# Optimization experiments

Hardware: AMD Instinct MI355X
Metric: run time of the kernel (lower is better)

The kernel has to match this reference:

```python
import jax, jax.numpy as jnp
import numpy as np

N_NODES = 200000
N_EDGES = 6400000
NUM_FEATURES = 128


def _glorot(key, fan_in, fan_out):
    return jax.random.normal(key, (fan_in, fan_out), jnp.float32) * (1.0 / np.sqrt(fan_in))


def gcn_conv(x, src, dst, W, b):
    """PyG GCNConv: h = D^{-1/2}(A+I)D^{-1/2} (x @ W) + b, self-loops added."""
    n = x.shape[0]
    ones = jnp.ones(src.shape, x.dtype)
    # degree after adding self-loops: 1 + in-degree (edges flow src -> dst)
    deg = 1.0 + jax.ops.segment_sum(ones, dst, num_segments=n)
    dinv = jax.lax.rsqrt(deg)  # deg >= 1, safe
    h = x @ W  # [n, out]
    norm = dinv[src] * dinv[dst]  # [E]
    msg = h[src] * norm[:, None]
    agg = jax.ops.segment_sum(msg, dst, num_segments=n)
    agg = agg + h * (dinv * dinv)[:, None]  # self-loop contribution
    return agg + b


def setup_inputs() -> dict:
    key = jax.random.key(0)
    ks = jax.random.split(key, 16)
    x = jax.random.normal(ks[0], (N_NODES, NUM_FEATURES), jnp.float32)
    edge_index = jax.random.randint(ks[1], (2, N_EDGES), 0, N_NODES, dtype=jnp.int64)
    params = {
        'W1': _glorot(ks[2], NUM_FEATURES, 64), 'b1': jnp.zeros((64,), jnp.float32),
        'W2': _glorot(ks[3], 64, 32),           'b2': jnp.zeros((32,), jnp.float32),
        'W3': _glorot(ks[4], 32, 16),           'b3': jnp.zeros((16,), jnp.float32),
        'Wsk02': _glorot(ks[5], NUM_FEATURES, 32), 'bsk02': jnp.zeros((32,), jnp.float32),
        'Wsk13': _glorot(ks[6], 64, 16),           'bsk13': jnp.zeros((16,), jnp.float32),
        'Wlin': _glorot(ks[7], 16, 1),             'blin': jnp.zeros((1,), jnp.float32),
    }
    return {'x': x, 'edge_index': edge_index, **params}


def reference(x, edge_index, W1, b1, W2, b2, W3, b3, Wsk02, bsk02, Wsk13, bsk13, Wlin, blin):
    # Dropout is identity in eval mode.
    src, dst = edge_index[0], edge_index[1]
    h1 = jax.nn.relu(gcn_conv(x, src, dst, W1, b1))
    h2 = jax.nn.relu(gcn_conv(h1, src, dst, W2, b2) + x @ Wsk02 + bsk02)
    h3 = jax.nn.relu(gcn_conv(h2, src, dst, W3, b3) + h1 @ Wsk13 + bsk13)
    return jax.nn.sigmoid(h3 @ Wlin + blin)  # [N, 1]
```

## Files before the change

### kernel.cpp

```cpp
#include <hip/hip_runtime.h>
#include <hip/hip_fp16.h>
#include <math.h>

#define MAXB 1024
#define MAXCB 128
#define TILE1 8192
#define SCAT_T 512
#define EPT1 (TILE1 / SCAT_T)
#define LCAP 13568

typedef _Float16 f16x8 __attribute__((ext_vector_type(8)));
typedef float f32x4 __attribute__((ext_vector_type(4)));


__device__ __forceinline__ unsigned int pack_f16(float a, float b) {
    __half2 h = __floats2half2_rn(a, b);
    return *reinterpret_cast<unsigned int*>(&h);
}
__device__ __forceinline__ float f16_lo(unsigned int u) {
    __half2 h = *reinterpret_cast<__half2*>(&u);
    return __low2float(h);
}
__device__ __forceinline__ float f16_hi(unsigned int u) {
    __half2 h = *reinterpret_cast<__half2*>(&u);
    return __high2float(h);
}
__device__ __forceinline__ void acc8(float* a, uint4 u) {
    a[0] += f16_lo(u.x); a[1] += f16_hi(u.x);
    a[2] += f16_lo(u.y); a[3] += f16_hi(u.y);
    a[4] += f16_lo(u.z); a[5] += f16_hi(u.z);
    a[6] += f16_lo(u.w); a[7] += f16_hi(u.w);
}
__device__ __forceinline__ void unpack8(uint4 u, float* v) {
    v[0] = f16_lo(u.x); v[1] = f16_hi(u.x);
    v[2] = f16_lo(u.y); v[3] = f16_hi(u.y);
    v[4] = f16_lo(u.z); v[5] = f16_hi(u.z);
    v[6] = f16_lo(u.w); v[7] = f16_hi(u.w);
}
__device__ __forceinline__ uint4 h2add4(uint4 a, uint4 b) {
    const __half2* pa = reinterpret_cast<const __half2*>(&a);
    const __half2* pb = reinterpret_cast<const __half2*>(&b);
    uint4 r;
    __half2* pr = reinterpret_cast<__half2*>(&r);
#pragma unroll
    for (int i = 0; i < 4; i++) pr[i] = __hadd2(pa[i], pb[i]);
    return r;
}


__device__ __forceinline__ bool detect64(const int* __restrict__ ei) {
    int lane = threadIdx.x & 63;
    unsigned long long m = __ballot(ei[2 * lane + 1] != 0);
    return m == 0ull;
}

__device__ __forceinline__ int load_src(const int* ei, int e, bool is64, int i) {
    return is64 ? ei[2 * i] : ei[i];
}
__device__ __forceinline__ int load_dst(const int* ei, int e, bool is64, int i) {
    return is64 ? ei[2 * e + 2 * i] : ei[e + i];
}


__global__ __launch_bounds__(256) void bin_count(const int* __restrict__ ei, int e,
                                                 int shift, int* __restrict__ gcnt) {
    __shared__ int h[MAXB];
    for (int i = threadIdx.x; i < MAXB; i += 256) h[i] = 0;
    bool is64 = detect64(ei);
    __syncthreads();
    int stride = gridDim.x * 256;
    for (int i = blockIdx.x * 256 + threadIdx.x; i < e; i += stride) {
        int d = load_dst(ei, e, is64, i);
        atomicAdd(&h[d >> shift], 1);
    }
    __syncthreads();
    for (int i = threadIdx.x; i < MAXB; i += 256)
        if (h[i]) atomicAdd(&gcnt[i], h[i]);
}


__global__ void bin_scan_init(const int* __restrict__ gcnt, int nb, int ncb,
                              int* __restrict__ base, int* __restrict__ gcursor,
                              int* __restrict__ gcur1) {
    __shared__ int sh[1024];
    __shared__ int ex[1024];
    int t = threadIdx.x;
    int v = (t < nb) ? gcnt[t] : 0;
    sh[t] = v;
    __syncthreads();
    for (int off = 1; off < 1024; off <<= 1) {
        int x = (t >= off) ? sh[t - off] : 0;
        __syncthreads();
        sh[t] += x;
        __syncthreads();
    }
    int excl = sh[t] - v;
    ex[t] = excl;
    if (t < nb) {
        base[t] = excl;
        gcursor[t] = excl;
        if (t == nb - 1) base[nb] = sh[t];
    }
    __syncthreads();
    if (t < ncb) gcur1[t] = ex[8 * t];
}


__global__ __launch_bounds__(SCAT_T) void scatter_coarse(const int* __restrict__ ei, int e,
                                                         int shift,
                                                         int* __restrict__ gcur1,
                                                         unsigned int* __restrict__ gpk1) {
    __shared__ int hist[MAXCB];
    __shared__ int lbase[MAXCB];
    __shared__ int delta[MAXCB];
    __shared__ int cur[MAXCB];
    __shared__ unsigned int sbuf[TILE1];
    __shared__ unsigned char sbkt[TILE1];
    __shared__ int sh[SCAT_T];

    const int t = threadIdx.x;
    const int pkshift = shift + 3;
    const int pkmask = (1 << pkshift) - 1;
    const bool is64 = detect64(ei);
    const int tile0 = blockIdx.x * TILE1;
    const int cnt = min(TILE1, e - tile0);

    for (int i = t; i < MAXCB; i += SCAT_T) hist[i] = 0;
    __syncthreads();

    unsigned int pk[EPT1];
    int bk[EPT1];
#pragma unroll
    for (int k = 0; k < EPT1; k++) {
        int g = tile0 + k * SCAT_T + t;
        bk[k] = -1;
        if (g < e) {
            int s = load_src(ei, e, is64, g);
            int d = load_dst(ei, e, is64, g);
            pk[k] = ((unsigned int)s << pkshift) | (unsigned int)(d & pkmask);
            bk[k] = d >> pkshift;
            atomicAdd(&hist[bk[k]], 1);
        }
    }
    __syncthreads();

    {
        int v = (t < MAXCB) ? hist[t] : 0;
        sh[t] = v;
        __syncthreads();
        for (int off = 1; off < SCAT_T; off <<= 1) {
            int x = (t >= off) ? sh[t - off] : 0;
            __syncthreads();
            sh[t] += x;
            __syncthreads();
        }
        if (t < MAXCB) lbase[t] = sh[t] - v;
    }
    __syncthreads();

    if (t < MAXCB) {
        int c = hist[t];
        if (c > 0) delta[t] = atomicAdd(&gcur1[t], c) - lbase[t];
        cur[t] = lbase[t];
    }
    __syncthreads();

#pragma unroll
    for (int k = 0; k < EPT1; k++) {
        if (bk[k] >= 0) {
            int p = atomicAdd(&cur[bk[k]], 1);
            sbuf[p] = pk[k];
            sbkt[p] = (unsigned char)bk[k];
        }
    }
    __syncthreads();

    for (int i = t; i < cnt; i += SCAT_T)
        gpk1[delta[sbkt[i]] + i] = sbuf[i];
}


__global__ __launch_bounds__(SCAT_T) void scatter_fine(const unsigned int* __restrict__ gpk1,
                                                       const int* __restrict__ base,
                                                       int nbkt, int shift,
                                                       int* __restrict__ gcursor,
                                                       unsigned int* __restrict__ gpk2) {
    __shared__ int hist[8];
    __shared__ int lbase[8];
    __shared__ int delta[8];
    __shared__ int cur[8];
    __shared__ unsigned int sbuf[TILE1];
    __shared__ unsigned char sbkt[TILE1];

    const int t = threadIdx.x;
    const int cb = blockIdx.x >> 3;
    const int s = blockIdx.x & 7;
    const int f0 = 8 * cb;
    const int fhiIdx = min(f0 + 8, nbkt);
    const int lo = base[f0];
    const int hi = base[fhiIdx];
    const int len = hi - lo;
    const int slo = lo + (int)((long long)len * s / 8);
    const int shi = lo + (int)((long long)len * (s + 1) / 8);

    for (int tile0 = slo; tile0 < shi; tile0 += TILE1) {
        const int cnt = min(TILE1, shi - tile0);
        if (t < 8) hist[t] = 0;
        __syncthreads();

        unsigned int pk[EPT1];
        int bk[EPT1];
#pragma unroll
        for (int k = 0; k < EPT1; k++) {
            int li = k * SCAT_T + t;
            bk[k] = -1;
            if (li < cnt) {
                pk[k] = gpk1[tile0 + li];
                bk[k] = (pk[k] >> shift) & 7;
                atomicAdd(&hist[bk[k]], 1);
            }
        }
        __syncthreads();

        if (t == 0) {
            int run = 0;
            for (int f = 0; f < 8; f++) { lbase[f] = run; run += hist[f]; }
        }
        __syncthreads();
        if (t < 8) {
            int c = hist[t];
            if (c > 0) delta[t] = atomicAdd(&gcursor[f0 + t], c) - lbase[t];
            cur[t] = lbase[t];
        }
        __syncthreads();

#pragma unroll
        for (int k = 0; k < EPT1; k++) {
            if (bk[k] >= 0) {
                int p = atomicAdd(&cur[bk[k]], 1);
                sbuf[p] = pk[k];
                sbkt[p] = (unsigned char)bk[k];
            }
        }
        __syncthreads();

        for (int i = t; i < cnt; i += SCAT_T)
            gpk2[delta[sbkt[i]] + i] = sbuf[i];
        __syncthreads();
    }
}


__global__ __launch_bounds__(256) void bucket_build(const unsigned int* __restrict__ gpk,
                                                    const int* __restrict__ base, int shift,
                                                    int n, int e, float* __restrict__ dinv,
                                                    int* __restrict__ row_ptr,
                                                    int* __restrict__ col) {
    __shared__ int lcol[LCAP];
    __shared__ int dc[MAXB];
    __shared__ int cur[MAXB];
    __shared__ int sh[256];
    const int t = threadIdx.x;
    const int b = blockIdx.x;
    const int pkshift = shift + 3;
    const int mask = (1 << shift) - 1;
    const int width = 1 << shift;
    const int node0 = b << shift;
    const int nc = min(width, n - node0);
    const int lo = base[b], hi = base[b + 1];
    const int ecnt = hi - lo;

    for (int i = t; i < width; i += 256) dc[i] = 0;
    __syncthreads();
    for (int j = lo + t; j < hi; j += 256)
        atomicAdd(&dc[gpk[j] & mask], 1);
    __syncthreads();
    {
        int b4 = t * 4;
        int v0 = (b4 + 0 < width) ? dc[b4 + 0] : 0;
        int v1 = (b4 + 1 < width) ? dc[b4 + 1] : 0;
        int v2 = (b4 + 2 < width) ? dc[b4 + 2] : 0;
        int v3 = (b4 + 3 < width) ? dc[b4 + 3] : 0;
        int s = v0 + v1 + v2 + v3;
        sh[t] = s;
        __syncthreads();
        for (int off = 1; off < 256; off <<= 1) {
            int x = (t >= off) ? sh[t - off] : 0;
            __syncthreads();
            sh[t] += x;
            __syncthreads();
        }
        int excl = sh[t] - s;
        int pf[4] = {excl, excl + v0, excl + v0 + v1, excl + v0 + v1 + v2};
        int vv[4] = {v0, v1, v2, v3};
#pragma unroll
        for (int q = 0; q < 4; q++) {
            int i = b4 + q;
            if (i < nc) {
                row_ptr[node0 + i] = lo + pf[q];
                dinv[node0 + i] = rsqrtf(1.0f + (float)vv[q]);
            }
            if (i < width) cur[i] = pf[q];
        }
    }
    if (b == gridDim.x - 1 && t == 0) row_ptr[n] = e;
    __syncthreads();

    if (ecnt <= LCAP) {
        for (int j = lo + t; j < hi; j += 256) {
            unsigned int v = gpk[j];
            int p = atomicAdd(&cur[v & mask], 1);
            lcol[p] = (int)(v >> pkshift);
        }
        __syncthreads();
        for (int j = t; j < ecnt; j += 256)
            col[lo + j] = lcol[j];
    } else {
        for (int j = lo + t; j < hi; j += 256) {
            unsigned int v = gpk[j];
            int p = atomicAdd(&cur[v & mask], 1);
            col[lo + p] = (int)(v >> pkshift);
        }
    }
}


__global__ void prep_w(const float* __restrict__ W1, const float* __restrict__ Wsk02,
                       const float* __restrict__ W2, const float* __restrict__ Wsk13,
                       const float* __restrict__ W3, unsigned short* __restrict__ wt) {
    int i = blockIdx.x * 256 + threadIdx.x;
    float v;
    if (i < 12288) {
        int c = i >> 7, k = i & 127;
        v = (c < 64) ? W1[k * 64 + c] : Wsk02[k * 32 + (c - 64)];
    } else if (i < 15360) {
        int j = i - 12288;
        int c = j >> 6, k = j & 63;
        v = (c < 32) ? W2[k * 32 + c] : Wsk13[k * 16 + (c - 32)];
    } else if (i < 15872) {
        int j = i - 15360;
        int c = j >> 5, k = j & 31;
        v = W3[k * 16 + c];
    } else return;
    wt[i] = (unsigned short)pack_f16(v, 0.f);
}


template <int K, int CO1, int CO2, bool AHALF>
__global__ __launch_bounds__(256) void gemm_mfma(const void* __restrict__ Av,
                                                 const unsigned short* __restrict__ wt,
                                                 const float* __restrict__ dinv,
                                                 unsigned int* __restrict__ out1,
                                                 float* __restrict__ out2, int n) {
    constexpr int N = CO1 + CO2;
    constexpr int NCT = N / 16;
    constexpr int NK = K / 32;
    constexpr int CHK = K / 8;
    constexpr int SWZ = (CHK - 1) < 15 ? (CHK - 1) : 15;
    __shared__ __align__(16) unsigned char Ash[64 * K * 2];
    __shared__ __align__(16) unsigned char Bsh[N * K * 2];

    const int t = threadIdx.x;
    const int row0 = blockIdx.x * 64;

    for (int i = t; i < 64 * CHK; i += 256) {
        int r = i / CHK, c = i % CHK;
        int row = row0 + r;
        uint4 w{0u, 0u, 0u, 0u};
        if (row < n) {
            if (AHALF) {
                w = *reinterpret_cast<const uint4*>(
                    (const unsigned short*)Av + (size_t)row * K + c * 8);
            } else {
                const float* xr = (const float*)Av + (size_t)row * K + c * 8;
                float4 p = *reinterpret_cast<const float4*>(xr);
                float4 q = *reinterpret_cast<const float4*>(xr + 4);
                w.x = pack_f16(p.x, p.y); w.y = pack_f16(p.z, p.w);
                w.z = pack_f16(q.x, q.y); w.w = pack_f16(q.z, q.w);
            }
        }
        int addr = i * 16;
        addr ^= ((r & SWZ) << 4);
        *reinterpret_cast<uint4*>(&Ash[addr]) = w;
    }
    for (int i = t; i < N * CHK; i += 256) {
        int cc = i / CHK;
        uint4 w = *reinterpret_cast<const uint4*>(&wt[(i / CHK) * K + (i % CHK) * 8]);
        int addr = i * 16;
        addr ^= ((cc & SWZ) << 4);
        *reinterpret_cast<uint4*>(&Bsh[addr]) = w;
    }
    __syncthreads();

    const int wv = t >> 6;
    const int lane = t & 63;
    const int lrow = wv * 16 + (lane & 15);
    const int kb = (lane >> 4) * 16;

    f16x8 afr[NK];
#pragma unroll
    for (int s = 0; s < NK; s++) {
        int addr = lrow * (2 * K) + s * 64 + kb;
        addr ^= ((lrow & SWZ) << 4);
        afr[s] = *reinterpret_cast<const f16x8*>(&Ash[addr]);
    }

    f32x4 acc[NCT];
#pragma unroll
    for (int ct = 0; ct < NCT; ct++) acc[ct] = f32x4{0.f, 0.f, 0.f, 0.f};

#pragma unroll
    for (int ct = 0; ct < NCT; ct++) {
        int cc = ct * 16 + (lane & 15);
#pragma unroll
        for (int s = 0; s < NK; s++) {
            int addr = cc * (2 * K) + s * 64 + kb;
            addr ^= ((cc & SWZ) << 4);
            f16x8 bfr = *reinterpret_cast<const f16x8*>(&Bsh[addr]);
            acc[ct] = __builtin_amdgcn_mfma_f32_16x16x32_f16(afr[s], bfr, acc[ct], 0, 0, 0);
        }
    }

    const int rbase = row0 + wv * 16 + (lane >> 4) * 4;
    const int cidx = lane & 15;
    float dn[4];
#pragma unroll
    for (int r = 0; r < 4; r++) dn[r] = (rbase + r < n) ? dinv[rbase + r] : 0.f;

#pragma unroll
    for (int ct = 0; ct < NCT; ct++) {
        int col = ct * 16 + cidx;
        if (col < CO1) {
#pragma unroll
            for (int r = 0; r < 4; r++) {
                float v = acc[ct][r] * dn[r];
                float o = __shfl_xor(v, 1);
                int row = rbase + r;
                if (!(lane & 1) && row < n)
                    out1[(size_t)row * (CO1 / 2) + ct * 8 + cidx / 2] = pack_f16(v, o);
            }
        } else if (CO2 > 0) {
#pragma unroll
            for (int r = 0; r < 4; r++) {
                int row = rbase + r;
                if (row < n) out2[(size_t)row * CO2 + (col - CO1)] = acc[ct][r];
            }
        }
    }
}


template <int F, bool FINAL, bool PACKOUT>
__global__ __launch_bounds__(256) void gather_combine(
    const uint4* __restrict__ hp4, const int* __restrict__ row_ptr,
    const int* __restrict__ col, const float* __restrict__ dinv,
    const float* __restrict__ bias, const float* __restrict__ sk,
    const float* __restrict__ bsk, void* __restrict__ outv,
    const float* __restrict__ Wlin, const float* __restrict__ blin, int n) {
    constexpr int L = F / 8;
    constexpr int EPW = 64 / L;
    int wid = (blockIdx.x * blockDim.x + threadIdx.x) >> 6;
    int lane = threadIdx.x & 63;
    if (wid >= n) return;
    int s = lane / L;
    int el = lane % L;
    int start = row_ptr[wid];
    int end = row_ptr[wid + 1];

    float a[8] = {0.f, 0.f, 0.f, 0.f, 0.f, 0.f, 0.f, 0.f};
    const uint4 z4{0u, 0u, 0u, 0u};
    for (int j = start + s; j < end; j += 4 * EPW) {
        int j1 = j + EPW, j2 = j + 2 * EPW, j3 = j + 3 * EPW;
        bool v1 = j1 < end, v2 = j2 < end, v3 = j3 < end;
        int c0 = col[j];
        int c1 = col[v1 ? j1 : j];
        int c2 = col[v2 ? j2 : j];
        int c3 = col[v3 ? j3 : j];
        uint4 u0 = hp4[(size_t)c0 * L + el];
        uint4 u1 = hp4[(size_t)c1 * L + el];
        uint4 u2 = hp4[(size_t)c2 * L + el];
        uint4 u3 = hp4[(size_t)c3 * L + el];
        if (!v1) u1 = z4;
        if (!v2) u2 = z4;
        if (!v3) u3 = z4;
        uint4 t01 = h2add4(u0, u1);
        uint4 t23 = h2add4(u2, u3);
        acc8(a, h2add4(t01, t23));
    }

#pragma unroll
    for (int m = L; m < 64; m <<= 1) {
#pragma unroll
        for (int q = 0; q < 8; q++) a[q] += __shfl_xor(a[q], m);
    }

    if (lane < L) {
        float dn = dinv[wid];
        uint4 us = hp4[(size_t)wid * L + el];
        float v[8];
        unpack8(us, v);
        float4 b0 = *reinterpret_cast<const float4*>(&bias[8 * el]);
        float4 b1 = *reinterpret_cast<const float4*>(&bias[8 * el + 4]);
        float o[8];
        o[0] = dn * a[0] + v[0] * dn + b0.x;
        o[1] = dn * a[1] + v[1] * dn + b0.y;
        o[2] = dn * a[2] + v[2] * dn + b0.z;
        o[3] = dn * a[3] + v[3] * dn + b0.w;
        o[4] = dn * a[4] + v[4] * dn + b1.x;
        o[5] = dn * a[5] + v[5] * dn + b1.y;
        o[6] = dn * a[6] + v[6] * dn + b1.z;
        o[7] = dn * a[7] + v[7] * dn + b1.w;
        if (sk) {
            float4 s0 = *reinterpret_cast<const float4*>(&sk[(size_t)wid * F + 8 * el]);
            float4 s1 = *reinterpret_cast<const float4*>(&sk[(size_t)wid * F + 8 * el + 4]);
            float4 k0 = *reinterpret_cast<const float4*>(&bsk[8 * el]);
            float4 k1 = *reinterpret_cast<const float4*>(&bsk[8 * el + 4]);
            o[0] += s0.x + k0.x; o[1] += s0.y + k0.y;
            o[2] += s0.z + k0.z; o[3] += s0.w + k0.w;
            o[4] += s1.x + k1.x; o[5] += s1.y + k1.y;
            o[6] += s1.z + k1.z; o[7] += s1.w + k1.w;
        }
#pragma unroll
        for (int q = 0; q < 8; q++) o[q] = fmaxf(o[q], 0.f);
        if (FINAL) {
            float4 wl0 = *reinterpret_cast<const float4*>(&Wlin[8 * el]);
            float4 wl1 = *reinterpret_cast<const float4*>(&Wlin[8 * el + 4]);
            float d = o[0] * wl0.x + o[1] * wl0.y + o[2] * wl0.z + o[3] * wl0.w +
                      o[4] * wl1.x + o[5] * wl1.y + o[6] * wl1.z + o[7] * wl1.w;
            d += __shfl_xor(d, 1);
            if (el == 0) ((float*)outv)[wid] = 1.0f / (1.0f + expf(-(d + blin[0])));
        } else if (PACKOUT) {
            uint4 pk{pack_f16(o[0], o[1]), pack_f16(o[2], o[3]),
                     pack_f16(o[4], o[5]), pack_f16(o[6], o[7])};
            ((uint4*)outv)[(size_t)wid * L + el] = pk;
        } else {
            float* out = (float*)outv;
            float4 w0{o[0], o[1], o[2], o[3]};
            float4 w1{o[4], o[5], o[6], o[7]};
            *reinterpret_cast<float4*>(&out[(size_t)wid * F + 8 * el]) = w0;
            *reinterpret_cast<float4*>(&out[(size_t)wid * F + 8 * el + 4]) = w1;
        }
    }
}


extern "C" void kernel_launch(void* const* d_in, const int* in_sizes, int n_in,
                              void* d_out, int out_size, void* d_ws, size_t ws_size,
                              hipStream_t stream) {
    const float* x     = (const float*)d_in[0];
    const int*   ei    = (const int*)d_in[1];
    const float* W1    = (const float*)d_in[2];
    const float* b1    = (const float*)d_in[3];
    const float* W2    = (const float*)d_in[4];
    const float* b2    = (const float*)d_in[5];
    const float* W3    = (const float*)d_in[6];
    const float* b3    = (const float*)d_in[7];
    const float* Wsk02 = (const float*)d_in[8];
    const float* bsk02 = (const float*)d_in[9];
    const float* Wsk13 = (const float*)d_in[10];
    const float* bsk13 = (const float*)d_in[11];
    const float* Wlin  = (const float*)d_in[12];
    const float* blin  = (const float*)d_in[13];

    const int n = in_sizes[0] / 128;
    const int e = in_sizes[1] / 2;

    int shift = 8;
    while (((n + (1 << shift) - 1) >> shift) > MAXB) shift++;
    const int nbkt = (n + (1 << shift) - 1) >> shift;
    const int ncb = (nbkt + 7) / 8;

    char* p = (char*)d_ws;
    auto alloc = [&](size_t bytes) {
        void* r = (void*)p;
        p += (bytes + 255) / 256 * 256;
        return r;
    };
    int*   gcnt    = (int*)alloc(MAXB * 4);
    int*   base    = (int*)alloc((MAXB + 1) * 4);
    int*   gcursor = (int*)alloc(MAXB * 4);
    int*   gcur1   = (int*)alloc(MAXCB * 4);
    unsigned short* wt = (unsigned short*)alloc(15872 * 2);
    int*   row_ptr = (int*)alloc((size_t)(n + 1) * 4);
    float* dinv    = (float*)alloc((size_t)n * 4);
    int*   col     = (int*)alloc((size_t)e * 4);
    size_t h1b     = (size_t)e * 4 > (size_t)n * 128 ? (size_t)e * 4 : (size_t)n * 128;
    unsigned int* h1 = (unsigned int*)alloc(h1b);
    unsigned int* h2 = (unsigned int*)alloc((size_t)n * 64);
    float* sk02    = (float*)alloc((size_t)n * 32 * 4);
    float* sk13    = (float*)alloc((size_t)n * 16 * 4);
    size_t prebytes = (size_t)e * 4 > (size_t)n * 128 ? (size_t)e * 4 : (size_t)n * 128;
    unsigned int* preb = (unsigned int*)alloc(prebytes);
    unsigned int* gpk1 = h1;
    unsigned int* gpk2 = preb;

    auto cdiv = [](int a, int b) { return (a + b - 1) / b; };

    prep_w<<<62, 256, 0, stream>>>(W1, Wsk02, W2, Wsk13, W3, wt);

    hipMemsetAsync(gcnt, 0, MAXB * 4, stream);
    bin_count<<<1024, 256, 0, stream>>>(ei, e, shift, gcnt);
    bin_scan_init<<<1, 1024, 0, stream>>>(gcnt, nbkt, ncb, base, gcursor, gcur1);
    scatter_coarse<<<cdiv(e, TILE1), SCAT_T, 0, stream>>>(ei, e, shift, gcur1, gpk1);
    scatter_fine<<<ncb * 8, SCAT_T, 0, stream>>>(gpk1, base, nbkt, shift, gcursor, gpk2);
    bucket_build<<<nbkt, 256, 0, stream>>>(gpk2, base, shift, n, e, dinv, row_ptr, col);

    gemm_mfma<128, 64, 32, false><<<cdiv(n, 64), 256, 0, stream>>>(
        x, wt, dinv, preb, sk02, n);
    gather_combine<64, false, true><<<cdiv(n, 4), 256, 0, stream>>>(
        (const uint4*)preb, row_ptr, col, dinv, b1, nullptr, nullptr, h1, nullptr, nullptr, n);

    gemm_mfma<64, 32, 16, true><<<cdiv(n, 64), 256, 0, stream>>>(
        h1, wt + 12288, dinv, preb, sk13, n);
    gather_combine<32, false, true><<<cdiv(n, 4), 256, 0, stream>>>(
        (const uint4*)preb, row_ptr, col, dinv, b2, sk02, bsk02, h2, nullptr, nullptr, n);

    gemm_mfma<32, 16, 0, true><<<cdiv(n, 64), 256, 0, stream>>>(
        h2, wt + 15360, dinv, preb, sk13, n);
    gather_combine<16, true, false><<<cdiv(n, 4), 256, 0, stream>>>(
        (const uint4*)preb, row_ptr, col, dinv, b3, sk13, bsk13, d_out, Wlin, blin, n);
}
```

Baseline: 516.8 us.

## Use thread-per-node gather with LDS-staged column indices for layers two and three

Adds a gather kernel that assigns one thread per destination node instead of a group of lanes, staging each block's CSR column indices in shared memory in chunks and accumulating neighbor rows with packed fp16 adds. It is used for the 32- and 16-feature layers, where the old lane-split scheme left many lanes idle per row. Accumulating in fp16 across ~32 neighbors lowers precision, and one thread per node creates load imbalance across a wavefront when degrees vary, plus uncoalesced per-thread row loads.

```diff
diff --git a/kernel.cpp b/kernel.cpp
--- a/kernel.cpp
+++ b/kernel.cpp
@@ -8,6 +8,7 @@
 #define SCAT_T 512
 #define EPT1 (TILE1 / SCAT_T)
 #define LCAP 13568
+#define GCHUNK 4096
 
 typedef _Float16 f16x8 __attribute__((ext_vector_type(8)));
 typedef float f32x4 __attribute__((ext_vector_type(4)));
@@ -45,6 +46,10 @@
 #pragma unroll
     for (int i = 0; i < 4; i++) pr[i] = __hadd2(pa[i], pb[i]);
     return r;
+}
+__device__ __forceinline__ unsigned int pkadd(unsigned int a, unsigned int b) {
+    __half2 r = __hadd2(*reinterpret_cast<__half2*>(&a), *reinterpret_cast<__half2*>(&b));
+    return *reinterpret_cast<unsigned int*>(&r);
 }
 
 
@@ -544,6 +549,97 @@
 }
 
 
+template <int F, bool FINAL, bool PACKOUT>
+__global__ __launch_bounds__(256) void gather_tpn(
+    const uint4* __restrict__ hp4, const int* __restrict__ row_ptr,
+    const int* __restrict__ col, const float* __restrict__ dinv,
+    const float* __restrict__ bias, const float* __restrict__ sk,
+    const float* __restrict__ bsk, void* __restrict__ outv,
+    const float* __restrict__ Wlin, const float* __restrict__ blin, int n) {
+    constexpr int L = F / 8;
+    __shared__ int lcol[GCHUNK];
+    const int t = threadIdx.x;
+    const int node0 = blockIdx.x * 256;
+    const int node = node0 + t;
+    const int hiN = min(node0 + 256, n);
+    const int lo = row_ptr[node0];
+    const int hi = row_ptr[hiN];
+
+    int start = 0, end = 0;
+    if (node < n) { start = row_ptr[node]; end = row_ptr[node + 1]; }
+
+    unsigned int acc[F / 2];
+#pragma unroll
+    for (int q = 0; q < F / 2; q++) acc[q] = 0u;
+
+    for (int ch = lo; ch < hi; ch += GCHUNK) {
+        int cnt = min(GCHUNK, hi - ch);
+        __syncthreads();
+        for (int i = t; i < cnt; i += 256) lcol[i] = col[ch + i];
+        __syncthreads();
+        int s0 = max(start, ch);
+        int s1 = min(end, ch + cnt);
+        for (int j = s0; j < s1; j++) {
+            int c = lcol[j - ch];
+            const uint4* rp = hp4 + (size_t)c * L;
+            uint4 u[L];
+#pragma unroll
+            for (int w = 0; w < L; w++) u[w] = rp[w];
+#pragma unroll
+            for (int w = 0; w < L; w++) {
+                acc[4 * w + 0] = pkadd(acc[4 * w + 0], u[w].x);
+                acc[4 * w + 1] = pkadd(acc[4 * w + 1], u[w].y);
+                acc[4 * w + 2] = pkadd(acc[4 * w + 2], u[w].z);
+                acc[4 * w + 3] = pkadd(acc[4 * w + 3], u[w].w);
+            }
+        }
+    }
+
+    if (node < n) {
+        float dn = dinv[node];
+        const uint4* sp = hp4 + (size_t)node * L;
+        float o[F];
+#pragma unroll
+        for (int w = 0; w < L; w++) {
+            uint4 u = sp[w];
+            float sv[8];
+            unpack8(u, sv);
+#pragma unroll
+            for (int q = 0; q < 8; q++) {
+                int f = w * 8 + q;
+                float av = (q & 1) ? f16_hi(acc[4 * w + (q >> 1)])
+                                   : f16_lo(acc[4 * w + (q >> 1)]);
+                o[f] = dn * (av + sv[q]) + bias[f];
+            }
+        }
+        if (sk) {
+#pragma unroll
+            for (int f = 0; f < F; f++)
+                o[f] += sk[(size_t)node * F + f] + bsk[f];
+        }
+#pragma unroll
+        for (int f = 0; f < F; f++) o[f] = fmaxf(o[f], 0.f);
+
+        if (FINAL) {
+            float d = blin[0];
+#pragma unroll
+            for (int f = 0; f < F; f++) d += o[f] * Wlin[f];
+            ((float*)outv)[node] = 1.0f / (1.0f + expf(-d));
+        } else if (PACKOUT) {
+            uint4* o4 = (uint4*)outv + (size_t)node * L;
+#pragma unroll
+            for (int w = 0; w < L; w++) {
+                uint4 pk{pack_f16(o[w * 8 + 0], o[w * 8 + 1]),
+                         pack_f16(o[w * 8 + 2], o[w * 8 + 3]),
+                         pack_f16(o[w * 8 + 4], o[w * 8 + 5]),
+                         pack_f16(o[w * 8 + 6], o[w * 8 + 7])};
+                o4[w] = pk;
+            }
+        }
+    }
+}
+
+
 extern "C" void kernel_launch(void* const* d_in, const int* in_sizes, int n_in,
                               void* d_out, int out_size, void* d_ws, size_t ws_size,
                               hipStream_t stream) {
@@ -612,11 +708,11 @@
 
     gemm_mfma<64, 32, 16, true><<<cdiv(n, 64), 256, 0, stream>>>(
         h1, wt + 12288, dinv, preb, sk13, n);
-    gather_combine<32, false, true><<<cdiv(n, 4), 256, 0, stream>>>(
+    gather_tpn<32, false, true><<<cdiv(n, 256), 256, 0, stream>>>(
         (const uint4*)preb, row_ptr, col, dinv, b2, sk02, bsk02, h2, nullptr, nullptr, n);
 
     gemm_mfma<32, 16, 0, true><<<cdiv(n, 64), 256, 0, stream>>>(
         h2, wt + 15360, dinv, preb, sk13, n);
-    gather_combine<16, true, false><<<cdiv(n, 4), 256, 0, stream>>>(
+    gather_tpn<16, true, false><<<cdiv(n, 256), 256, 0, stream>>>(
         (const uint4*)preb, row_ptr, col, dinv, b3, sk13, bsk13, d_out, Wlin, blin, n);
 }
```

Measured after the change: 532.2 us. 3.0% more time.
